# Optimization experiments

Hardware: AMD Instinct MI355X
Metric: run time of the kernel (lower is better)

The kernel has to match this reference:

```python
import jax, jax.numpy as jnp
import numpy as np

B, At, Nbr = 4, 1024, 32
Fn, Fe, L = 128, 128, 3
N_TYPES = 100
G_END = 5.5  # gaussian_filter_end = cutoff - 0.5
ZIN = 2 * Fn + Fe


def setup_inputs() -> dict:
    key = jax.random.key(0)
    ks = jax.random.split(key, 16)
    s = lambda fan: 1.0 / np.sqrt(fan)
    inp = {}
    inp["Z"] = jax.random.randint(ks[0], (B, At), 0, N_TYPES)
    inp["nbr_idx"] = jax.random.randint(ks[1], (B, At, Nbr), 0, At)
    inp["distances"] = jax.random.uniform(ks[2], (B, At, Nbr), jnp.float32) * 6.0
    inp["unit_vecs"] = jax.random.normal(ks[3], (B, At, Nbr, 3), jnp.float32)
    # learned parameters
    inp["emb_table"] = jax.random.normal(ks[4], (N_TYPES, Fn), jnp.float32)
    inp["Wnf"] = jax.random.normal(ks[5], (L, ZIN, Fn), jnp.float32) * s(ZIN)
    inp["bnf"] = jnp.zeros((L, Fn), jnp.float32)
    inp["Wnc"] = jax.random.normal(ks[6], (L, ZIN, Fn), jnp.float32) * s(ZIN)
    inp["bnc"] = jnp.zeros((L, Fn), jnp.float32)
    inp["Wef"] = jax.random.normal(ks[7], (L, ZIN, Fe), jnp.float32) * s(ZIN)
    inp["bef"] = jnp.zeros((L, Fe), jnp.float32)
    inp["Wec"] = jax.random.normal(ks[8], (L, ZIN, Fe), jnp.float32) * s(ZIN)
    inp["bec"] = jnp.zeros((L, Fe), jnp.float32)
    # ForceMagnitudeMapping: 2 output layers, softplus on hidden, none on last
    inp["Wo1"] = jax.random.normal(ks[9], (Fe, Fe // 2), jnp.float32) * s(Fe)
    inp["bo1"] = jnp.zeros((Fe // 2,), jnp.float32)
    inp["Wo2"] = jax.random.normal(ks[10], (Fe // 2, 1), jnp.float32) * s(Fe // 2)
    inp["bo2"] = jnp.zeros((1,), jnp.float32)
    return inp


def _gather_nbr(h, nbr_idx):
    # h: [B, At, F], nbr_idx: [B, At, Nbr] -> [B, At, Nbr, F]
    b, at, f = h.shape
    nbr = nbr_idx.shape[-1]
    idx = nbr_idx.reshape(b, at * nbr, 1)
    return jnp.take_along_axis(h, idx, axis=1).reshape(b, at, nbr, f)


def reference(Z, nbr_idx, distances, unit_vecs, emb_table,
              Wnf, bnf, Wnc, bnc, Wef, bef, Wec, bec,
              Wo1, bo1, Wo2, bo2):
    # Gaussian filter of neighbor distances -> initial edge embedding [B,At,Nbr,Fe]
    mu = jnp.linspace(0.0, G_END, Fe)
    coeff = -0.5 / (mu[1] - mu[0]) ** 2
    e = jnp.exp(coeff * (distances[..., None] - mu) ** 2)
    # node embedding lookup [B,At,Fn]
    h = emb_table[Z]
    for l in range(L):
        # node update: gated (CGCNN-style) aggregation over neighbor edges
        hj = _gather_nbr(h, nbr_idx)
        hi = jnp.broadcast_to(h[:, :, None, :], hj.shape)
        z = jnp.concatenate([hi, hj, e], axis=-1)  # [B,At,Nbr,2Fn+Fe]
        msg = jax.nn.sigmoid(z @ Wnf[l] + bnf[l]) * jax.nn.softplus(z @ Wnc[l] + bnc[l])
        h = h + msg.sum(axis=2)
        # edge update from the freshly updated endpoint node features
        hj2 = _gather_nbr(h, nbr_idx)
        hi2 = jnp.broadcast_to(h[:, :, None, :], hj2.shape)
        z2 = jnp.concatenate([hi2, hj2, e], axis=-1)
        e = e + jax.nn.sigmoid(z2 @ Wef[l] + bef[l]) * jax.nn.softplus(z2 @ Wec[l] + bec[l])
    # force-magnitude mapping: softplus hidden, linear last -> [B,At,Nbr,1]
    fm = jax.nn.softplus(e @ Wo1 + bo1) @ Wo2 + bo2
    # expand over xyz, weight by unit vectors, reduce over neighbors
    forces = (fm * unit_vecs).sum(axis=2)  # [B,At,3]
    return forces
```

## Files before the change

kernel.cpp:

```cpp
#include <hip/hip_runtime.h>
#include <math.h>

#define AT 1024
#define NBR 32
#define FN 128
#define FE 128
#define ZIN 384
#define NA 4096
#define NEDGE (NA * NBR)
#define WSTRIDE (ZIN * FN)
#define G_ENDF 5.5f
#define WTMAT (384 * 128)
#define EPART (256 * 128)

typedef unsigned short ushort_t;
typedef __attribute__((ext_vector_type(8))) short bf16x8;
typedef __attribute__((ext_vector_type(4))) float f32x4;

#define LOG2E 1.4426950408889634f
#define LN2   0.6931471805599453f

__device__ __forceinline__ float fexp(float x) {
    return __builtin_amdgcn_exp2f(x * LOG2E);
}
__device__ __forceinline__ float sigmoid_f(float x) {
    return __builtin_amdgcn_rcpf(1.0f + __builtin_amdgcn_exp2f(-x * LOG2E));
}
__device__ __forceinline__ float softplus_f(float x) {
    float t = __builtin_amdgcn_exp2f(-fabsf(x) * LOG2E);
    return fmaxf(x, 0.0f) + LN2 * __builtin_amdgcn_logf(1.0f + t);
}

__device__ __forceinline__ ushort_t f2bf(float f) {
    unsigned int u = __float_as_uint(f);
    u = (u + 0x7FFFu + ((u >> 16) & 1u)) >> 16;
    return (ushort_t)u;
}
__device__ __forceinline__ float bf2f(ushort_t h) {
    return __uint_as_float(((unsigned int)h) << 16);
}
__device__ __forceinline__ unsigned int cvt_pk_bf16(float a, float b) {
    unsigned int r;
    asm("v_cvt_pk_bf16_f32 %0, %1, %2" : "=v"(r) : "v"(a), "v"(b));
    return r;
}
__device__ __forceinline__ void split2(float a, float b,
                                       unsigned int& hi, unsigned int& lo) {
    hi = cvt_pk_bf16(a, b);
    float ha = __uint_as_float(hi << 16);
    float hb = __uint_as_float(hi & 0xffff0000u);
    lo = cvt_pk_bf16(a - ha, b - hb);
}

__global__ __launch_bounds__(256) void k_init_h(const int* __restrict__ Z,
                                                const float* __restrict__ emb,
                                                float* __restrict__ h) {
    int idx = blockIdx.x * 256 + threadIdx.x;
    int atom = idx >> 7, f = idx & 127;
    h[idx] = emb[Z[atom] * FN + f];
}

__global__ __launch_bounds__(256) void k_conv_w(const float* __restrict__ Wnf,
                                                const float* __restrict__ Wnc,
                                                const float* __restrict__ Wef,
                                                const float* __restrict__ Wec,
                                                ushort_t* __restrict__ Whi,
                                                ushort_t* __restrict__ Wlo) {
    const int blk = blockIdx.x;
    const int w = blk / 3, p = blk % 3;
    const int l = w >> 2, t = w & 3;
    const float* src = (t == 0 ? Wnf : t == 1 ? Wnc : t == 2 ? Wef : Wec)
                       + (size_t)l * WSTRIDE + (size_t)p * 128 * 128;
    __shared__ float tile[128][129];
    const int tid = threadIdx.x;
    {
        int k = tid >> 1, h = (tid & 1) * 64;
#pragma unroll
        for (int i = 0; i < 16; ++i) {
            float4 v = *(const float4*)&src[k * 128 + h + i * 4];
            tile[k][h + i * 4 + 0] = v.x; tile[k][h + i * 4 + 1] = v.y;
            tile[k][h + i * 4 + 2] = v.z; tile[k][h + i * 4 + 3] = v.w;
        }
    }
    __syncthreads();
    {
        int f = tid >> 1, kh = (tid & 1) * 64;
        size_t orow = (size_t)(w * 384 + p * 128 + f) * 128;
#pragma unroll
        for (int i = 0; i < 64; i += 4) {
            ushort4 ph, pl;
            float x0 = tile[kh + i + 0][f]; ph.x = f2bf(x0); pl.x = f2bf(x0 - bf2f(ph.x));
            float x1 = tile[kh + i + 1][f]; ph.y = f2bf(x1); pl.y = f2bf(x1 - bf2f(ph.y));
            float x2 = tile[kh + i + 2][f]; ph.z = f2bf(x2); pl.z = f2bf(x2 - bf2f(ph.z));
            float x3 = tile[kh + i + 3][f]; ph.w = f2bf(x3); pl.w = f2bf(x3 - bf2f(ph.w));
            *(ushort4*)&Whi[orow + kh + i] = ph;
            *(ushort4*)&Wlo[orow + kh + i] = pl;
        }
    }
}

__global__ __launch_bounds__(256) void k_conv_wo(const float* __restrict__ Wo1,
                                                 ushort_t* __restrict__ Wh,
                                                 ushort_t* __restrict__ Wl) {
    int idx = blockIdx.x * 256 + threadIdx.x;
    int n = idx >> 7, k = idx & 127;
    float x = Wo1[k * 64 + n];
    ushort_t h = f2bf(x);
    Wh[idx] = h;
    Wl[idx] = f2bf(x - bf2f(h));
}

__global__ __launch_bounds__(512, 4) void k_proj(
    const float* __restrict__ h,
    const ushort_t* __restrict__ Wah, const ushort_t* __restrict__ Wal,
    const ushort_t* __restrict__ Wbh, const ushort_t* __restrict__ Wbl,
    const float* __restrict__ ba, const float* __restrict__ bb,
    float* __restrict__ Pai, float* __restrict__ Paj,
    float* __restrict__ Pbi, float* __restrict__ Pbj) {
    const int tid = threadIdx.x;
    const int a0 = blockIdx.x * 16;
    __shared__ __align__(16) ushort_t sAh[16 * 136];
    __shared__ __align__(16) ushort_t sAl[16 * 136];
    {
        int row = tid >> 5, kq = (tid & 31) * 4;
        float4 v = *(const float4*)&h[(size_t)(a0 + row) * 128 + kq];
        unsigned int h0, l0, h1, l1;
        split2(v.x, v.y, h0, l0);
        split2(v.z, v.w, h1, l1);
        *(uint2*)&sAh[row * 136 + kq] = make_uint2(h0, h1);
        *(uint2*)&sAl[row * 136 + kq] = make_uint2(l0, l1);
    }
    __syncthreads();

    const int w = tid >> 6;
    const int lane = tid & 63;
    const int lrow = lane & 15;
    const int kgrp = (lane >> 4) * 8;

    f32x4 acc[4] = {};
#pragma unroll
    for (int kk = 0; kk < 4; ++kk) {
        const int kbase = kk * 32 + kgrp;
        bf16x8 ah = *(const bf16x8*)&sAh[lrow * 136 + kbase];
        bf16x8 al = *(const bf16x8*)&sAl[lrow * 136 + kbase];
#pragma unroll
        for (int nt = 0; nt < 4; ++nt) {
            int r512 = w * 64 + nt * 16 + lrow;
            const ushort_t* bh_p = (r512 < 256) ? (Wah + (size_t)r512 * 128)
                                                : (Wbh + (size_t)(r512 - 256) * 128);
            const ushort_t* bl_p = (r512 < 256) ? (Wal + (size_t)r512 * 128)
                                                : (Wbl + (size_t)(r512 - 256) * 128);
            bf16x8 bh = *(const bf16x8*)&bh_p[kbase];
            bf16x8 bl = *(const bf16x8*)&bl_p[kbase];
            acc[nt] = __builtin_amdgcn_mfma_f32_16x16x32_bf16(ah, bh, acc[nt], 0, 0, 0);
            acc[nt] = __builtin_amdgcn_mfma_f32_16x16x32_bf16(ah, bl, acc[nt], 0, 0, 0);
            acc[nt] = __builtin_amdgcn_mfma_f32_16x16x32_bf16(al, bh, acc[nt], 0, 0, 0);
        }
    }

    const int arr = w >> 1;
    float* dst = (arr == 0) ? Pai : (arr == 1) ? Paj : (arr == 2) ? Pbi : Pbj;
    const int rb = (lane >> 4) * 4;
#pragma unroll
    for (int nt = 0; nt < 4; ++nt) {
        int f = (w & 1) * 64 + nt * 16 + lrow;
        float bs = (arr == 0) ? ba[f] : (arr == 2) ? bb[f] : 0.0f;
#pragma unroll
        for (int r = 0; r < 4; ++r) {
            int row = rb + r;
            dst[(size_t)(a0 + row) * 128 + f] = acc[nt][r] + bs;
        }
    }
}

template <int NODE, int FIRST, int FUSE>
__global__ __launch_bounds__(512, 4) void k_pass(
    const float* __restrict__ e_g, float* __restrict__ e_out,
    const float* __restrict__ dist, const int* __restrict__ nbr,
    const float* __restrict__ Pfi, const float* __restrict__ Pfj,
    const float* __restrict__ Pci, const float* __restrict__ Pcj,
    const ushort_t* __restrict__ Wfh, const ushort_t* __restrict__ Wfl,
    const ushort_t* __restrict__ Wch, const ushort_t* __restrict__ Wcl,
    const float* __restrict__ h_old, float* __restrict__ h_new,
    const ushort_t* __restrict__ Wo1h, const ushort_t* __restrict__ Wo1l,
    const float* __restrict__ bo1, const float* __restrict__ Wo2,
    const float* __restrict__ bo2, const float* __restrict__ unit,
    float* __restrict__ out) {
    const int tid = threadIdx.x;
    const int a0 = blockIdx.x * 2;
    const int base = (a0 >> 10) << 10;

    __shared__ __align__(16) ushort_t sAh[64 * 136];
    __shared__ __align__(16) ushort_t sAl[64 * 136];
    __shared__ int snbr[64];
    __shared__ float sred[4][64];

    {
        int row = tid >> 3, kq = (tid & 7) * 16;
        size_t eoff = ((size_t)(a0 * 32 + row)) * 128 + kq;
        float v[16];
        if (FIRST) {
            const float delta = G_ENDF / 127.0f;
            const float coeff = -0.5f / (delta * delta);
            float d = dist[a0 * 32 + row];
#pragma unroll
            for (int i = 0; i < 16; ++i) {
                float x = d - (float)(kq + i) * delta;
                v[i] = fexp(coeff * x * x);
            }
#pragma unroll
            for (int i = 0; i < 4; ++i)
                *(float4*)&e_out[eoff + i * 4] =
                    make_float4(v[i * 4], v[i * 4 + 1], v[i * 4 + 2], v[i * 4 + 3]);
        } else {
#pragma unroll
            for (int i = 0; i < 4; ++i) {
                float4 t = *(const float4*)&e_g[eoff + i * 4];
                v[i * 4] = t.x; v[i * 4 + 1] = t.y; v[i * 4 + 2] = t.z; v[i * 4 + 3] = t.w;
            }
        }
#pragma unroll
        for (int i = 0; i < 4; ++i) {
            unsigned int h0, l0, h1, l1;
            split2(v[i * 4 + 0], v[i * 4 + 1], h0, l0);
            split2(v[i * 4 + 2], v[i * 4 + 3], h1, l1);
            *(uint2*)&sAh[row * 136 + kq + i * 4] = make_uint2(h0, h1);
            *(uint2*)&sAl[row * 136 + kq + i * 4] = make_uint2(l0, l1);
        }
    }
    if (tid < 64) snbr[tid] = nbr[a0 * 32 + tid];
    __syncthreads();

    const int w = tid >> 6;
    const int lane = tid & 63;
    const int wr = w >> 2;
    const int wc = w & 3;
    const int lrow = lane & 15;
    const int kgrp = (lane >> 4) * 8;
    const int rb = (lane >> 4) * 4;

    f32x4 accf[2][2] = {};
    f32x4 accc[2][2] = {};

#pragma unroll
    for (int kk = 0; kk < 4; ++kk) {
        const int kbase = kk * 32 + kgrp;
        bf16x8 ah[2], al[2];
#pragma unroll
        for (int mt = 0; mt < 2; ++mt) {
            ah[mt] = *(const bf16x8*)&sAh[(wr * 32 + mt * 16 + lrow) * 136 + kbase];
            al[mt] = *(const bf16x8*)&sAl[(wr * 32 + mt * 16 + lrow) * 136 + kbase];
        }
#pragma unroll
        for (int nt = 0; nt < 2; ++nt) {
            const int nn = wc * 32 + nt * 16 + lrow;
            bf16x8 bfh = *(const bf16x8*)&Wfh[(size_t)nn * 128 + kbase];
            bf16x8 bfl = *(const bf16x8*)&Wfl[(size_t)nn * 128 + kbase];
            bf16x8 bch = *(const bf16x8*)&Wch[(size_t)nn * 128 + kbase];
            bf16x8 bcl = *(const bf16x8*)&Wcl[(size_t)nn * 128 + kbase];
#pragma unroll
            for (int mt = 0; mt < 2; ++mt) {
                accf[mt][nt] = __builtin_amdgcn_mfma_f32_16x16x32_bf16(ah[mt], bfh, accf[mt][nt], 0, 0, 0);
                accf[mt][nt] = __builtin_amdgcn_mfma_f32_16x16x32_bf16(ah[mt], bfl, accf[mt][nt], 0, 0, 0);
                accf[mt][nt] = __builtin_amdgcn_mfma_f32_16x16x32_bf16(al[mt], bfh, accf[mt][nt], 0, 0, 0);
                accc[mt][nt] = __builtin_amdgcn_mfma_f32_16x16x32_bf16(ah[mt], bch, accc[mt][nt], 0, 0, 0);
                accc[mt][nt] = __builtin_amdgcn_mfma_f32_16x16x32_bf16(ah[mt], bcl, accc[mt][nt], 0, 0, 0);
                accc[mt][nt] = __builtin_amdgcn_mfma_f32_16x16x32_bf16(al[mt], bch, accc[mt][nt], 0, 0, 0);
            }
        }
    }

    if (FUSE) __syncthreads();

    float hsum[2] = {0.0f, 0.0f};
#pragma unroll
    for (int nt = 0; nt < 2; ++nt) {
        const int nn = wc * 32 + nt * 16 + lrow;
        const float pfi = Pfi[(size_t)(a0 + wr) * 128 + nn];
        const float pci = Pci[(size_t)(a0 + wr) * 128 + nn];
#pragma unroll
        for (int mt = 0; mt < 2; ++mt) {
#pragma unroll
            for (int r = 0; r < 4; ++r) {
                const int rl = wr * 32 + mt * 16 + rb + r;
                const int j = base + snbr[rl];
                float cf = accf[mt][nt][r] + pfi + Pfj[(size_t)j * 128 + nn];
                float cc = accc[mt][nt][r] + pci + Pcj[(size_t)j * 128 + nn];
                float msg = sigmoid_f(cf) * softplus_f(cc);
                if (NODE) {
                    hsum[nt] += msg;
                } else {
                    size_t eo = ((size_t)(a0 * 32 + rl)) * 128 + nn;
                    float enew = e_g[eo] + msg;
                    if (FUSE) {
                        ushort_t hh = f2bf(enew);
                        sAh[rl * 136 + nn] = hh;
                        sAl[rl * 136 + nn] = f2bf(enew - bf2f(hh));
                    } else {
                        e_out[eo] = enew;
                    }
                }
            }
        }
    }

    if (NODE) {
#pragma unroll
        for (int nt = 0; nt < 2; ++nt) {
            float v = hsum[nt];
            v += __shfl_xor(v, 16, 64);
            v += __shfl_xor(v, 32, 64);
            if (lane < 16) {
                int col = wc * 32 + nt * 16 + lane;
                h_new[(size_t)(a0 + wr) * 128 + col] =
                    h_old[(size_t)(a0 + wr) * 128 + col] + v;
            }
        }
    }

    if (FUSE) {
        __syncthreads();
        f32x4 acco[2] = {};
        const int col = wc * 16 + lrow;
#pragma unroll
        for (int kk = 0; kk < 4; ++kk) {
            const int kbase = kk * 32 + kgrp;
            bf16x8 bh = *(const bf16x8*)&Wo1h[(size_t)col * 128 + kbase];
            bf16x8 bl = *(const bf16x8*)&Wo1l[(size_t)col * 128 + kbase];
#pragma unroll
            for (int mt = 0; mt < 2; ++mt) {
                bf16x8 ah = *(const bf16x8*)&sAh[(wr * 32 + mt * 16 + lrow) * 136 + kbase];
                bf16x8 al = *(const bf16x8*)&sAl[(wr * 32 + mt * 16 + lrow) * 136 + kbase];
                acco[mt] = __builtin_amdgcn_mfma_f32_16x16x32_bf16(ah, bh, acco[mt], 0, 0, 0);
                acco[mt] = __builtin_amdgcn_mfma_f32_16x16x32_bf16(ah, bl, acco[mt], 0, 0, 0);
                acco[mt] = __builtin_amdgcn_mfma_f32_16x16x32_bf16(al, bh, acco[mt], 0, 0, 0);
            }
        }
        const float b1 = bo1[col];
        const float w2 = Wo2[col];
#pragma unroll
        for (int mt = 0; mt < 2; ++mt) {
#pragma unroll
            for (int r = 0; r < 4; ++r) {
                float val = softplus_f(acco[mt][r] + b1) * w2;
                val += __shfl_xor(val, 1, 64);
                val += __shfl_xor(val, 2, 64);
                val += __shfl_xor(val, 4, 64);
                val += __shfl_xor(val, 8, 64);
                if (lrow == 0) sred[wc][wr * 32 + mt * 16 + rb + r] = val;
            }
        }
        __syncthreads();
        if (tid < 6) {
            int a = (tid < 3) ? 0 : 1;
            int c = tid - a * 3;
            float b2 = bo2[0];
            float s = 0.0f;
#pragma unroll 4
            for (int n = 0; n < 32; ++n) {
                int row = a * 32 + n;
                float fm = sred[0][row] + sred[1][row] + sred[2][row] + sred[3][row] + b2;
                s += fm * unit[((size_t)((a0 + a) * 32 + n)) * 3 + c];
            }
            out[(size_t)(a0 + a) * 3 + c] = s;
        }
    }
}

extern "C" void kernel_launch(void* const* d_in, const int* in_sizes, int n_in,
                              void* d_out, int out_size, void* d_ws, size_t ws_size,
                              hipStream_t stream) {
    const int*   Z    = (const int*)d_in[0];
    const int*   nbr  = (const int*)d_in[1];
    const float* dist = (const float*)d_in[2];
    const float* unit = (const float*)d_in[3];
    const float* emb  = (const float*)d_in[4];
    const float* Wnf  = (const float*)d_in[5];
    const float* bnf  = (const float*)d_in[6];
    const float* Wnc  = (const float*)d_in[7];
    const float* bnc  = (const float*)d_in[8];
    const float* Wef  = (const float*)d_in[9];
    const float* bef  = (const float*)d_in[10];
    const float* Wec  = (const float*)d_in[11];
    const float* bec  = (const float*)d_in[12];
    const float* Wo1  = (const float*)d_in[13];
    const float* bo1  = (const float*)d_in[14];
    const float* Wo2  = (const float*)d_in[15];
    const float* bo2  = (const float*)d_in[16];
    float* out = (float*)d_out;

    float* ws = (float*)d_ws;
    float* e   = ws;
    float* h0  = e + (size_t)NEDGE * FE;
    float* h1  = h0 + (size_t)NA * FN;
    float* Pfi = h1 + (size_t)NA * FN;
    float* Pfj = Pfi + (size_t)NA * FN;
    float* Pci = Pfj + (size_t)NA * FN;
    float* Pcj = Pci + (size_t)NA * FN;
    ushort_t* Whi  = (ushort_t*)(Pcj + (size_t)NA * FN);
    ushort_t* Wlo  = Whi + (size_t)12 * WTMAT;
    ushort_t* Wo1h = Wlo + (size_t)12 * WTMAT;
    ushort_t* Wo1l = Wo1h + (size_t)64 * 128;

    k_conv_w<<<36, 256, 0, stream>>>(Wnf, Wnc, Wef, Wec, Whi, Wlo);
    k_conv_wo<<<32, 256, 0, stream>>>(Wo1, Wo1h, Wo1l);
    k_init_h<<<(NA * FN) / 256, 256, 0, stream>>>(Z, emb, h0);

    float* hc = h0;
    float* hn = h1;
    for (int l = 0; l < 3; ++l) {
        const ushort_t* nf_h = Whi + (size_t)(l * 4 + 0) * WTMAT;
        const ushort_t* nf_l = Wlo + (size_t)(l * 4 + 0) * WTMAT;
        const ushort_t* nc_h = Whi + (size_t)(l * 4 + 1) * WTMAT;
        const ushort_t* nc_l = Wlo + (size_t)(l * 4 + 1) * WTMAT;
        const ushort_t* ef_h = Whi + (size_t)(l * 4 + 2) * WTMAT;
        const ushort_t* ef_l = Wlo + (size_t)(l * 4 + 2) * WTMAT;
        const ushort_t* ec_h = Whi + (size_t)(l * 4 + 3) * WTMAT;
        const ushort_t* ec_l = Wlo + (size_t)(l * 4 + 3) * WTMAT;

        k_proj<<<NA / 16, 512, 0, stream>>>(hc, nf_h, nf_l, nc_h, nc_l,
                                            bnf + l * FN, bnc + l * FN,
                                            Pfi, Pfj, Pci, Pcj);
        if (l == 0)
            k_pass<1, 1, 0><<<NA / 2, 512, 0, stream>>>(
                e, e, dist, nbr, Pfi, Pfj, Pci, Pcj,
                nf_h + EPART, nf_l + EPART, nc_h + EPART, nc_l + EPART,
                hc, hn, nullptr, nullptr, nullptr, nullptr, nullptr, nullptr, nullptr);
        else
            k_pass<1, 0, 0><<<NA / 2, 512, 0, stream>>>(
                e, e, dist, nbr, Pfi, Pfj, Pci, Pcj,
                nf_h + EPART, nf_l + EPART, nc_h + EPART, nc_l + EPART,
                hc, hn, nullptr, nullptr, nullptr, nullptr, nullptr, nullptr, nullptr);

        k_proj<<<NA / 16, 512, 0, stream>>>(hn, ef_h, ef_l, ec_h, ec_l,
                                            bef + l * FN, bec + l * FN,
                                            Pfi, Pfj, Pci, Pcj);
        if (l < 2)
            k_pass<0, 0, 0><<<NA / 2, 512, 0, stream>>>(
                e, e, dist, nbr, Pfi, Pfj, Pci, Pcj,
                ef_h + EPART, ef_l + EPART, ec_h + EPART, ec_l + EPART,
                nullptr, nullptr, nullptr, nullptr, nullptr, nullptr, nullptr, nullptr, nullptr);
        else
            k_pass<0, 0, 1><<<NA / 2, 512, 0, stream>>>(
                e, e, dist, nbr, Pfi, Pfj, Pci, Pcj,
                ef_h + EPART, ef_l + EPART, ec_h + EPART, ec_l + EPART,
                nullptr, nullptr, Wo1h, Wo1l, bo1, Wo2, bo2, unit, out);

        float* t = hc; hc = hn; hn = t;
    }
}
```

Baseline: 678.1 us.

## Interleave filter/core projections and prefetch neighbor gathers before MFMA loop

The four per-node projection arrays become two interleaved arrays holding (filter, core) pairs, so each neighbor gather is one float2 load instead of two scalar loads. These gathers and the self-projection loads are issued before the MFMA loop so their latency can overlap the matrix work. The old edge value is now rebuilt from the hi/lo bf16 split already in shared memory instead of being re-read from global memory. This costs 18 more float2 registers per thread, which may hurt occupancy. Reconstructing e from bf16 hi+lo is also slightly less precise than the original fp32 value.

```diff
diff --git a/kernel.cpp b/kernel.cpp
--- a/kernel.cpp
+++ b/kernel.cpp
@@ -115,8 +115,7 @@
     const ushort_t* __restrict__ Wah, const ushort_t* __restrict__ Wal,
     const ushort_t* __restrict__ Wbh, const ushort_t* __restrict__ Wbl,
     const float* __restrict__ ba, const float* __restrict__ bb,
-    float* __restrict__ Pai, float* __restrict__ Paj,
-    float* __restrict__ Pbi, float* __restrict__ Pbj) {
+    float* __restrict__ Pi, float* __restrict__ Pj) {
     const int tid = threadIdx.x;
     const int a0 = blockIdx.x * 16;
     __shared__ __align__(16) ushort_t sAh[16 * 136];
@@ -159,7 +158,8 @@
     }
 
     const int arr = w >> 1;
-    float* dst = (arr == 0) ? Pai : (arr == 1) ? Paj : (arr == 2) ? Pbi : Pbj;
+    float* dst = (arr & 1) ? Pj : Pi;
+    const int slot = arr >> 1;
     const int rb = (lane >> 4) * 4;
 #pragma unroll
     for (int nt = 0; nt < 4; ++nt) {
@@ -168,7 +168,7 @@
 #pragma unroll
         for (int r = 0; r < 4; ++r) {
             int row = rb + r;
-            dst[(size_t)(a0 + row) * 128 + f] = acc[nt][r] + bs;
+            dst[((size_t)(a0 + row) * 128 + f) * 2 + slot] = acc[nt][r] + bs;
         }
     }
 }
@@ -177,8 +177,7 @@
 __global__ __launch_bounds__(512, 4) void k_pass(
     const float* __restrict__ e_g, float* __restrict__ e_out,
     const float* __restrict__ dist, const int* __restrict__ nbr,
-    const float* __restrict__ Pfi, const float* __restrict__ Pfj,
-    const float* __restrict__ Pci, const float* __restrict__ Pcj,
+    const float* __restrict__ Pi, const float* __restrict__ Pj,
     const ushort_t* __restrict__ Wfh, const ushort_t* __restrict__ Wfl,
     const ushort_t* __restrict__ Wch, const ushort_t* __restrict__ Wcl,
     const float* __restrict__ h_old, float* __restrict__ h_new,
@@ -239,6 +238,22 @@
     const int kgrp = (lane >> 4) * 8;
     const int rb = (lane >> 4) * 4;
 
+    float2 pi_[2];
+    float2 pj_[2][8];
+#pragma unroll
+    for (int nt = 0; nt < 2; ++nt) {
+        const int nn = wc * 32 + nt * 16 + lrow;
+        pi_[nt] = *(const float2*)&Pi[((size_t)(a0 + wr) * 128 + nn) * 2];
+#pragma unroll
+        for (int mt = 0; mt < 2; ++mt)
+#pragma unroll
+            for (int r = 0; r < 4; ++r) {
+                const int rl = wr * 32 + mt * 16 + rb + r;
+                const int j = base + snbr[rl];
+                pj_[nt][mt * 4 + r] = *(const float2*)&Pj[((size_t)j * 128 + nn) * 2];
+            }
+    }
+
     f32x4 accf[2][2] = {};
     f32x4 accc[2][2] = {};
 
@@ -276,28 +291,27 @@
 #pragma unroll
     for (int nt = 0; nt < 2; ++nt) {
         const int nn = wc * 32 + nt * 16 + lrow;
-        const float pfi = Pfi[(size_t)(a0 + wr) * 128 + nn];
-        const float pci = Pci[(size_t)(a0 + wr) * 128 + nn];
 #pragma unroll
         for (int mt = 0; mt < 2; ++mt) {
 #pragma unroll
             for (int r = 0; r < 4; ++r) {
                 const int rl = wr * 32 + mt * 16 + rb + r;
-                const int j = base + snbr[rl];
-                float cf = accf[mt][nt][r] + pfi + Pfj[(size_t)j * 128 + nn];
-                float cc = accc[mt][nt][r] + pci + Pcj[(size_t)j * 128 + nn];
+                const int idx = mt * 4 + r;
+                float cf = accf[mt][nt][r] + pi_[nt].x + pj_[nt][idx].x;
+                float cc = accc[mt][nt][r] + pi_[nt].y + pj_[nt][idx].y;
                 float msg = sigmoid_f(cf) * softplus_f(cc);
                 if (NODE) {
                     hsum[nt] += msg;
                 } else {
-                    size_t eo = ((size_t)(a0 * 32 + rl)) * 128 + nn;
-                    float enew = e_g[eo] + msg;
+                    const int lidx = rl * 136 + nn;
+                    float eold = bf2f(sAh[lidx]) + bf2f(sAl[lidx]);
+                    float enew = eold + msg;
                     if (FUSE) {
                         ushort_t hh = f2bf(enew);
-                        sAh[rl * 136 + nn] = hh;
-                        sAl[rl * 136 + nn] = f2bf(enew - bf2f(hh));
+                        sAh[lidx] = hh;
+                        sAl[lidx] = f2bf(enew - bf2f(hh));
                     } else {
-                        e_out[eo] = enew;
+                        e_out[((size_t)(a0 * 32 + rl)) * 128 + nn] = enew;
                     }
                 }
             }
@@ -393,11 +407,9 @@
     float* e   = ws;
     float* h0  = e + (size_t)NEDGE * FE;
     float* h1  = h0 + (size_t)NA * FN;
-    float* Pfi = h1 + (size_t)NA * FN;
-    float* Pfj = Pfi + (size_t)NA * FN;
-    float* Pci = Pfj + (size_t)NA * FN;
-    float* Pcj = Pci + (size_t)NA * FN;
-    ushort_t* Whi  = (ushort_t*)(Pcj + (size_t)NA * FN);
+    float* Pi  = h1 + (size_t)NA * FN;
+    float* Pj  = Pi + (size_t)NA * FN * 2;
+    ushort_t* Whi  = (ushort_t*)(Pj + (size_t)NA * FN * 2);
     ushort_t* Wlo  = Whi + (size_t)12 * WTMAT;
     ushort_t* Wo1h = Wlo + (size_t)12 * WTMAT;
     ushort_t* Wo1l = Wo1h + (size_t)64 * 128;
@@ -419,30 +431,28 @@
         const ushort_t* ec_l = Wlo + (size_t)(l * 4 + 3) * WTMAT;
 
         k_proj<<<NA / 16, 512, 0, stream>>>(hc, nf_h, nf_l, nc_h, nc_l,
-                                            bnf + l * FN, bnc + l * FN,
-                                            Pfi, Pfj, Pci, Pcj);
+                                            bnf + l * FN, bnc + l * FN, Pi, Pj);
         if (l == 0)
             k_pass<1, 1, 0><<<NA / 2, 512, 0, stream>>>(
-                e, e, dist, nbr, Pfi, Pfj, Pci, Pcj,
+                e, e, dist, nbr, Pi, Pj,
                 nf_h + EPART, nf_l + EPART, nc_h + EPART, nc_l + EPART,
                 hc, hn, nullptr, nullptr, nullptr, nullptr, nullptr, nullptr, nullptr);
         else
             k_pass<1, 0, 0><<<NA / 2, 512, 0, stream>>>(
-                e, e, dist, nbr, Pfi, Pfj, Pci, Pcj,
+                e, e, dist, nbr, Pi, Pj,
                 nf_h + EPART, nf_l + EPART, nc_h + EPART, nc_l + EPART,
                 hc, hn, nullptr, nullptr, nullptr, nullptr, nullptr, nullptr, nullptr);
 
         k_proj<<<NA / 16, 512, 0, stream>>>(hn, ef_h, ef_l, ec_h, ec_l,
-                                            bef + l * FN, bec + l * FN,
-                                            Pfi, Pfj, Pci, Pcj);
+                                            bef + l * FN, bec + l * FN, Pi, Pj);
         if (l < 2)
             k_pass<0, 0, 0><<<NA / 2, 512, 0, stream>>>(
-                e, e, dist, nbr, Pfi, Pfj, Pci, Pcj,
+                e, e, dist, nbr, Pi, Pj,
                 ef_h + EPART, ef_l + EPART, ec_h + EPART, ec_l + EPART,
                 nullptr, nullptr, nullptr, nullptr, nullptr, nullptr, nullptr, nullptr, nullptr);
         else
             k_pass<0, 0, 1><<<NA / 2, 512, 0, stream>>>(
-                e, e, dist, nbr, Pfi, Pfj, Pci, Pcj,
+                e, e, dist, nbr, Pi, Pj,
                 ef_h + EPART, ef_l + EPART, ec_h + EPART, ec_l + EPART,
                 nullptr, nullptr, Wo1h, Wo1l, bo1, Wo2, bo2, unit, out);
 
```

New measurement: 672.3 us. About the same (-0.9%).
